# Optimization experiments

Measured on AMD Instinct MI355X. Metric: run time of the kernel, lower is better.

Reference implementation:

```python
import jax, jax.numpy as jnp
import numpy as np

M, N, D = 4, 65536, 256

def setup_inputs() -> dict:
    key = jax.random.key(0)
    k1, k2, k3 = jax.random.split(key, 3)
    x = jax.random.normal(k1, (M, N, D), dtype=jnp.float32)
    # W[i,j] is the (out,in) weight of fusion_layers[i][j]; b[i,j] its bias.
    W = jax.random.normal(k2, (M, M, D, D), dtype=jnp.float32) * (1.0 / np.sqrt(D))
    b = jax.random.normal(k3, (M, M, D), dtype=jnp.float32) * 0.02
    return {"x": x, "W": W, "b": b}

def reference(x, W, b):
    # x: [M, N, D] stacked modality features (zip(*features) rows vectorized over N)
    # out[i] = x[i] + sum_{j != i} (x[j] @ W[i,j]^T + b[i,j])
    m = x.shape[0]
    mask = (1.0 - jnp.eye(m)).astype(x.dtype)            # zero on diagonal (skip i==j)
    y = jnp.einsum('ijef,jnf->ijne', W, x) + b[:, :, None, :]  # [M, M, N, D]
    out = x + jnp.einsum('ij,ijne->ine', mask, y)         # fused masked accumulation
    return out
```

## Files before the change

### kernel.cpp

```cpp
#include <hip/hip_runtime.h>
#include <hip/hip_bf16.h>
#include <stdint.h>

#define NN 65536
#define DD 256

typedef uint32_t u32;
typedef __attribute__((ext_vector_type(4))) float f32x4;
typedef __attribute__((ext_vector_type(4))) u32 u32x4;
typedef __attribute__((ext_vector_type(2))) u32 u32x2;
typedef __attribute__((ext_vector_type(8))) short s16x8;

__device__ inline unsigned short f2bf(float f) {
    union { float f; u32 u; } v; v.f = f;
    u32 u = v.u;
    return (unsigned short)((u + 0x7fffu + ((u >> 16) & 1u)) >> 16);
}

__device__ inline void gl2lds16(const void* g, void* s) {
    __builtin_amdgcn_global_load_lds(
        (const __attribute__((address_space(1))) void*)g,
        (__attribute__((address_space(3))) void*)s, 16, 0, 0);
}

__global__ void prep_w256(const float* __restrict__ W, unsigned short* __restrict__ Wimg) {
    int t = blockIdx.x * blockDim.x + threadIdx.x;
    int E = t * 4;
    int tile = E >> 14;
    int pin = E & 16383;
    int col = pin >> 6;
    int r2e = pin & 63;
    int ct = tile >> 4;
    int j = (tile >> 2) & 3;
    int kk = tile & 3;
    int kl = r2e ^ ((col & 7) << 3);
    int i = ct;
    int e = col;
    int f = kk * 64 + kl;
    u32 p0, p1;
    if (i == j) {
        unsigned short d0 = (e == f + 0) ? 0x3F80 : 0;
        unsigned short d1 = (e == f + 1) ? 0x3F80 : 0;
        unsigned short d2 = (e == f + 2) ? 0x3F80 : 0;
        unsigned short d3 = (e == f + 3) ? 0x3F80 : 0;
        p0 = (u32)d0 | ((u32)d1 << 16);
        p1 = (u32)d2 | ((u32)d3 << 16);
    } else {
        f32x4 w = *(const f32x4*)(W + ((size_t)((i * 4 + j) * 256 + e) << 8) + f);
        p0 = (u32)f2bf(w[0]) | ((u32)f2bf(w[1]) << 16);
        p1 = (u32)f2bf(w[2]) | ((u32)f2bf(w[3]) << 16);
    }
    u32x2 pr = {p0, p1};
    *(u32x2*)(Wimg + E) = pr;
}

__global__ void prep_w128(const float* __restrict__ W, unsigned short* __restrict__ Wimg) {
    int t = blockIdx.x * blockDim.x + threadIdx.x;
    int E = t * 4;
    int tile = E >> 13;
    int pin = E & 8191;
    int col = pin >> 6;
    int r2e = pin & 63;
    int ct = tile >> 4;
    int j = (tile >> 2) & 3;
    int kk = tile & 3;
    int kl = r2e ^ ((col & 7) << 3);
    int c = ct * 128 + col;
    int i = c >> 8, e = c & 255;
    int f = kk * 64 + kl;
    u32 p0, p1;
    if (i == j) {
        p0 = 0u; p1 = 0u;
    } else {
        f32x4 w = *(const f32x4*)(W + ((size_t)((i * 4 + j) * 256 + e) << 8) + f);
        p0 = (u32)f2bf(w[0]) | ((u32)f2bf(w[1]) << 16);
        p1 = (u32)f2bf(w[2]) | ((u32)f2bf(w[3]) << 16);
    }
    u32x2 pr = {p0, p1};
    *(u32x2*)(Wimg + E) = pr;
}

__global__ void prep_x(const float* __restrict__ x, unsigned short* __restrict__ Ximg) {
    int t = blockIdx.x * blockDim.x + threadIdx.x;
    long long E = (long long)t * 4;
    int tile = (int)(E >> 14);
    int pin = (int)(E & 16383);
    int row = pin >> 6;
    int r2e = pin & 63;
    int kk = tile & 3;
    int rt = (tile >> 2) & 255;
    int j = tile >> 10;
    int kl = r2e ^ ((row & 7) << 3);
    int n = rt * 256 + row;
    int f = kk * 64 + kl;
    f32x4 v = *(const f32x4*)(x + ((size_t)j * NN + n) * DD + f);
    u32 p0 = (u32)f2bf(v[0]) | ((u32)f2bf(v[1]) << 16);
    u32 p1 = (u32)f2bf(v[2]) | ((u32)f2bf(v[3]) << 16);
    u32x2 pr = {p0, p1};
    *(u32x2*)(Ximg + E) = pr;
}

__global__ void prep_b(const float* __restrict__ b, float* __restrict__ bsum) {
    int c = blockIdx.x * blockDim.x + threadIdx.x;
    if (c >= 1024) return;
    int i = c >> 8, e = c & 255;
    float s = 0.0f;
    #pragma unroll
    for (int j = 0; j < 4; ++j)
        if (j != i) s += b[((i * 4 + j) << 8) + e];
    bsum[c] = s;
}

__global__ __launch_bounds__(512, 2) void fusion_gemm6(
    const unsigned short* __restrict__ Wimg, const unsigned short* __restrict__ Ximg,
    const float* __restrict__ bsum, float* __restrict__ out) {
    __shared__ __attribute__((aligned(16))) char lds[2][65536];

    const int tid = threadIdx.x;
    const int bid = blockIdx.x;
    const int xcd = bid & 7;
    const int slot = bid >> 3;
    const int ct = slot & 3;
    const int rhi = slot >> 2;
    const int rtile = rhi * 8 + xcd;
    const int n0 = rtile * 256;
    const int col0 = ct * 256;

    const int lane = tid & 63;
    const int wid = tid >> 6;
    const int wm = wid & 1;
    const int wn = wid >> 1;

    f32x4 acc[8][4];
    #pragma unroll
    for (int a = 0; a < 8; ++a)
        #pragma unroll
        for (int b2 = 0; b2 < 4; ++b2)
            acc[a][b2] = (f32x4){0.f, 0.f, 0.f, 0.f};

    const char* WimgB = (const char*)Wimg;
    const char* XimgB = (const char*)Ximg;
    const u32 loff = (u32)(wid * 1024);
    const u32 goff = (u32)(wid * 1024 + lane * 16);

    s16x8 fA0[2][4], fA1[2][4];
    s16x8 fB0[2][2], fB1[2][2];

#define STAGE_TILE(t_, D_)                                                            \
    {                                                                                 \
        int j_ = (t_) >> 2;                                                           \
        int kk_ = (t_) & 3;                                                           \
        const char* as_ = XimgB + (((size_t)((j_ * 256 + rtile) * 4 + kk_)) << 15) + goff; \
        const char* bs_ = WimgB + (((size_t)((ct * 4 + j_) * 4 + kk_)) << 15) + goff; \
        _Pragma("unroll")                                                             \
        for (int q = 0; q < 4; ++q) {                                                 \
            gl2lds16(as_ + q * 8192, (D_) + q * 8192 + loff);                         \
            gl2lds16(bs_ + q * 8192, (D_) + 32768 + q * 8192 + loff);                 \
        }                                                                             \
    }

#define RD_A(BUF_, mh_, SET_)                                                         \
    _Pragma("unroll")                                                                 \
    for (int kh = 0; kh < 2; ++kh) {                                                  \
        _Pragma("unroll")                                                             \
        for (int fm = 0; fm < 4; ++fm) {                                              \
            int r_ = wm * 128 + ((mh_) * 4 + fm) * 16 + (lane & 15);                  \
            u32 o_ = (u32)(r_ * 128 + kh * 64 + (lane >> 4) * 16);                    \
            o_ ^= (u32)((r_ & 7) << 4);                                               \
            SET_[kh][fm] = *(const s16x8*)((BUF_) + o_);                              \
        }                                                                             \
    }

#define RD_B(BUF_, nh_, SET_)                                                         \
    _Pragma("unroll")                                                                 \
    for (int kh = 0; kh < 2; ++kh) {                                                  \
        _Pragma("unroll")                                                             \
        for (int fn = 0; fn < 2; ++fn) {                                              \
            int c_ = wn * 64 + ((nh_) * 2 + fn) * 16 + (lane & 15);                   \
            u32 o_ = (u32)(c_ * 128 + kh * 64 + (lane >> 4) * 16);                    \
            o_ ^= (u32)((c_ & 7) << 4);                                               \
            SET_[kh][fn] = *(const s16x8*)((BUF_) + 32768 + o_);                      \
        }                                                                             \
    }

#define MM(AS_, BS_, mh_, nh_)                                                        \
    _Pragma("unroll")                                                                 \
    for (int kh = 0; kh < 2; ++kh) {                                                  \
        _Pragma("unroll")                                                             \
        for (int fm = 0; fm < 4; ++fm) {                                              \
            _Pragma("unroll")                                                         \
            for (int fn = 0; fn < 2; ++fn) {                                          \
                acc[(mh_) * 4 + fm][(nh_) * 2 + fn] =                                 \
                    __builtin_amdgcn_mfma_f32_16x16x32_bf16(                          \
                        AS_[kh][fm], BS_[kh][fn],                                     \
                        acc[(mh_) * 4 + fm][(nh_) * 2 + fn], 0, 0, 0);                \
            }                                                                         \
        }                                                                             \
    }

    STAGE_TILE(0, lds[0]);
    asm volatile("s_waitcnt vmcnt(0)" ::: "memory");
    __builtin_amdgcn_s_barrier();

    #pragma unroll 1
    for (int t = 0; t < 16; ++t) {
        const char* Bf = lds[t & 1];
        char* Of = lds[(t + 1) & 1];

        if (t < 15) STAGE_TILE(t + 1, Of);

        RD_A(Bf, 0, fA0);
        RD_B(Bf, 0, fB0);
        __builtin_amdgcn_s_setprio(1);
        MM(fA0, fB0, 0, 0);
        RD_B(Bf, 1, fB1);
        MM(fA0, fB1, 0, 1);
        RD_A(Bf, 1, fA1);
        MM(fA1, fB1, 1, 1);
        MM(fA1, fB0, 1, 0);
        __builtin_amdgcn_s_setprio(0);

        asm volatile("s_waitcnt vmcnt(0)" ::: "memory");
        __builtin_amdgcn_s_barrier();
    }

#undef STAGE_TILE
#undef RD_A
#undef RD_B
#undef MM

    const int r0 = (lane >> 4) * 4;
    const int cl = lane & 15;
    #pragma unroll
    for (int mf = 0; mf < 8; ++mf) {
        #pragma unroll
        for (int nf = 0; nf < 4; ++nf) {
            int col_l = wn * 64 + nf * 16 + cl;
            float bs = bsum[col0 + col_l];
            #pragma unroll
            for (int r = 0; r < 4; ++r) {
                int n = n0 + wm * 128 + mf * 16 + r0 + r;
                size_t oidx = ((size_t)ct * NN + n) * DD + col_l;
                out[oidx] = acc[mf][nf][r] + bs;
            }
        }
    }
}

__global__ __launch_bounds__(256, 2) void fusion_gemm_fb(
    const float* __restrict__ x, const unsigned short* __restrict__ Wimg,
    const float* __restrict__ bsum, float* __restrict__ out) {
    __shared__ __attribute__((aligned(16))) unsigned short Alds[128 * 64];
    __shared__ __attribute__((aligned(16))) unsigned short Blds[2][128 * 64];

    const int tid = threadIdx.x;
    const int bid = blockIdx.x;
    const int xcd = bid & 7;
    const int slot = bid >> 3;
    const int ct = slot & 7;
    const int rhi = slot >> 3;
    const int rtile = rhi * 8 + xcd;
    const int n0 = rtile * 128;
    const int col0 = ct * 128;
    const int i = ct >> 1;

    const int lane = tid & 63;
    const int wid = tid >> 6;
    const int wm = wid >> 1;
    const int wn = wid & 1;

    f32x4 acc[4][4];
    #pragma unroll
    for (int a = 0; a < 4; ++a)
        #pragma unroll
        for (int b2 = 0; b2 < 4; ++b2)
            acc[a][b2] = (f32x4){0.f, 0.f, 0.f, 0.f};

    const int sr = tid >> 1;
    const int sh = tid & 1;
    char* Ab = (char*)Alds;
    const char* WimgB = (const char*)Wimg;

    f32x4 av[8];
    {
        int j0 = (i == 0) ? 1 : 0;
        const float* asrc = x + (size_t)j0 * ((size_t)NN * DD) + (size_t)(n0 + sr) * DD + sh * 32;
        #pragma unroll
        for (int q = 0; q < 8; ++q) av[q] = *(const f32x4*)(asrc + q * 4);
        const char* base = WimgB + (((size_t)(ct * 4 + j0) * 4 + 0) << 14) + wid * 1024 + lane * 16;
        char* lb = (char*)Blds[0] + wid * 1024;
        #pragma unroll
        for (int q = 0; q < 4; ++q) gl2lds16(base + q * 4096, lb + q * 4096);
    }

    for (int t = 0; t < 12; ++t) {
        __syncthreads();
        #pragma unroll
        for (int q = 0; q < 4; ++q) {
            f32x4 v0 = av[2 * q], v1 = av[2 * q + 1];
            u32x4 p;
            p[0] = (u32)f2bf(v0[0]) | ((u32)f2bf(v0[1]) << 16);
            p[1] = (u32)f2bf(v0[2]) | ((u32)f2bf(v0[3]) << 16);
            p[2] = (u32)f2bf(v1[0]) | ((u32)f2bf(v1[1]) << 16);
            p[3] = (u32)f2bf(v1[2]) | ((u32)f2bf(v1[3]) << 16);
            u32 o = (u32)(sr * 128 + sh * 64 + q * 16);
            o ^= (u32)((sr & 7) << 4);
            *(u32x4*)(Ab + o) = p;
        }
        __syncthreads();

        if (t < 11) {
            int tn = t + 1;
            int jjn = tn >> 2;
            int jn = jjn + (jjn >= i);
            int kkn = tn & 3;
            const char* base = WimgB + (((size_t)(ct * 4 + jn) * 4 + kkn) << 14) + wid * 1024 + lane * 16;
            char* lb = (char*)Blds[tn & 1] + wid * 1024;
            #pragma unroll
            for (int q = 0; q < 4; ++q) gl2lds16(base + q * 4096, lb + q * 4096);
            const float* asrc = x + (size_t)jn * ((size_t)NN * DD) + (size_t)(n0 + sr) * DD + kkn * 64 + sh * 32;
            #pragma unroll
            for (int q = 0; q < 8; ++q) av[q] = *(const f32x4*)(asrc + q * 4);
        }

        const char* Bb = (const char*)Blds[t & 1];
        #pragma unroll
        for (int kh = 0; kh < 2; ++kh) {
            s16x8 af[4], bfr[4];
            #pragma unroll
            for (int fm = 0; fm < 4; ++fm) {
                int row = wm * 64 + fm * 16 + (lane & 15);
                u32 o = (u32)(row * 128 + kh * 64 + (lane >> 4) * 16);
                o ^= (u32)((row & 7) << 4);
                af[fm] = *(const s16x8*)(Ab + o);
            }
            #pragma unroll
            for (int fn = 0; fn < 4; ++fn) {
                int col = wn * 64 + fn * 16 + (lane & 15);
                u32 o = (u32)(col * 128 + kh * 64 + (lane >> 4) * 16);
                o ^= (u32)((col & 7) << 4);
                bfr[fn] = *(const s16x8*)(Bb + o);
            }
            #pragma unroll
            for (int fm = 0; fm < 4; ++fm)
                #pragma unroll
                for (int fn = 0; fn < 4; ++fn)
                    acc[fm][fn] = __builtin_amdgcn_mfma_f32_16x16x32_bf16(
                        af[fm], bfr[fn], acc[fm][fn], 0, 0, 0);
        }
    }

    const int r0 = (lane >> 4) * 4;
    const int cl = lane & 15;
    #pragma unroll
    for (int fm = 0; fm < 4; ++fm) {
        #pragma unroll
        for (int fn = 0; fn < 4; ++fn) {
            int col_l = wn * 64 + fn * 16 + cl;
            int cglob = col0 + col_l;
            float bs = bsum[cglob];
            int e = cglob & 255;
            #pragma unroll
            for (int r = 0; r < 4; ++r) {
                int row_l = wm * 64 + fm * 16 + r0 + r;
                int n = n0 + row_l;
                size_t oidx = ((size_t)i * NN + n) * DD + e;
                out[oidx] = acc[fm][fn][r] + x[oidx] + bs;
            }
        }
    }
}

extern "C" void kernel_launch(void* const* d_in, const int* in_sizes, int n_in,
                              void* d_out, int out_size, void* d_ws, size_t ws_size,
                              hipStream_t stream) {
    const float* x = (const float*)d_in[0];
    const float* W = (const float*)d_in[1];
    const float* b = (const float*)d_in[2];
    float* out = (float*)d_out;

    unsigned short* Wimg = (unsigned short*)d_ws;
    float* bsum = (float*)((char*)d_ws + ((size_t)8 << 20));
    const size_t ximg_off = (size_t)9 << 20;
    const size_t need = ximg_off + ((size_t)128 << 20);

    if (ws_size >= need) {
        unsigned short* Ximg = (unsigned short*)((char*)d_ws + ximg_off);
        hipLaunchKernelGGL(prep_b, dim3(4), dim3(256), 0, stream, b, bsum);
        hipLaunchKernelGGL(prep_w256, dim3(1024), dim3(256), 0, stream, W, Wimg);
        hipLaunchKernelGGL(prep_x, dim3(65536), dim3(256), 0, stream, x, Ximg);
        hipLaunchKernelGGL(fusion_gemm6, dim3(1024), dim3(512), 0, stream, Wimg, Ximg, bsum, out);
    } else {
        float* bsum2 = (float*)((char*)d_ws + ((size_t)2 << 20));
        hipLaunchKernelGGL(prep_b, dim3(4), dim3(256), 0, stream, b, bsum2);
        hipLaunchKernelGGL(prep_w128, dim3(1024), dim3(256), 0, stream, W, Wimg);
        hipLaunchKernelGGL(fusion_gemm_fb, dim3(4096), dim3(256), 0, stream, x, Wimg, bsum2, out);
    }
}
```

Before: 257.7 us.

## Interleave split A/B staging with MFMA clusters and fine-grained barriers

Splits the global-to-LDS tile staging into separate A and B loads and issues them after the corresponding LDS fragment reads, interleaved with four MFMA clusters per k-step. Adds explicit lgkmcnt waits, sched_barriers and workgroup barriers between clusters so the warps march in lockstep, in the style of a ping-pong schedule. The aim is to spread memory issue across the compute phase and keep the MFMA pipes fed. In exchange it adds more barriers per iteration, which can cost synchronisation stalls. Most of the time goes to the prep kernels, so a gain in the GEMM may be diluted.

After: 267.8 us. +3.9%, slower.

```diff
diff --git a/kernel.cpp b/kernel.cpp
--- a/kernel.cpp
+++ b/kernel.cpp
@@ -111,7 +111,7 @@
     bsum[c] = s;
 }
 
-__global__ __launch_bounds__(512, 2) void fusion_gemm6(
+__global__ __launch_bounds__(512, 2) void fusion_gemm8(
     const unsigned short* __restrict__ Wimg, const unsigned short* __restrict__ Ximg,
     const float* __restrict__ bsum, float* __restrict__ out) {
     __shared__ __attribute__((aligned(16))) char lds[2][65536];
@@ -146,17 +146,24 @@
     s16x8 fA0[2][4], fA1[2][4];
     s16x8 fB0[2][2], fB1[2][2];
 
-#define STAGE_TILE(t_, D_)                                                            \
+#define STAGE_A(t_, D_)                                                               \
     {                                                                                 \
         int j_ = (t_) >> 2;                                                           \
         int kk_ = (t_) & 3;                                                           \
         const char* as_ = XimgB + (((size_t)((j_ * 256 + rtile) * 4 + kk_)) << 15) + goff; \
+        _Pragma("unroll")                                                             \
+        for (int q = 0; q < 4; ++q)                                                   \
+            gl2lds16(as_ + q * 8192, (D_) + q * 8192 + loff);                         \
+    }
+
+#define STAGE_B(t_, D_)                                                               \
+    {                                                                                 \
+        int j_ = (t_) >> 2;                                                           \
+        int kk_ = (t_) & 3;                                                           \
         const char* bs_ = WimgB + (((size_t)((ct * 4 + j_) * 4 + kk_)) << 15) + goff; \
         _Pragma("unroll")                                                             \
-        for (int q = 0; q < 4; ++q) {                                                 \
-            gl2lds16(as_ + q * 8192, (D_) + q * 8192 + loff);                         \
+        for (int q = 0; q < 4; ++q)                                                   \
             gl2lds16(bs_ + q * 8192, (D_) + 32768 + q * 8192 + loff);                 \
-        }                                                                             \
     }
 
 #define RD_A(BUF_, mh_, SET_)                                                         \
@@ -198,36 +205,62 @@
         }                                                                             \
     }
 
-    STAGE_TILE(0, lds[0]);
-    asm volatile("s_waitcnt vmcnt(0)" ::: "memory");
-    __builtin_amdgcn_s_barrier();
+#define SB  __builtin_amdgcn_sched_barrier(0)
+#define BAR __builtin_amdgcn_s_barrier()
+#define LGKM(n_) asm volatile("s_waitcnt lgkmcnt(" #n_ ")" ::: "memory")
+#define VM0 asm volatile("s_waitcnt vmcnt(0)" ::: "memory")
+#define CLUSTER(AS_, BS_, mh_, nh_)                                                   \
+    __builtin_amdgcn_s_setprio(1);                                                    \
+    MM(AS_, BS_, mh_, nh_);                                                           \
+    __builtin_amdgcn_s_setprio(0);                                                    \
+    SB;                                                                               \
+    BAR;
+
+    STAGE_A(0, lds[0]);
+    STAGE_B(0, lds[0]);
+    VM0;
+    BAR;
 
     #pragma unroll 1
     for (int t = 0; t < 16; ++t) {
         const char* Bf = lds[t & 1];
         char* Of = lds[(t + 1) & 1];
 
-        if (t < 15) STAGE_TILE(t + 1, Of);
-
         RD_A(Bf, 0, fA0);
         RD_B(Bf, 0, fB0);
-        __builtin_amdgcn_s_setprio(1);
-        MM(fA0, fB0, 0, 0);
+        if (t < 15) STAGE_A(t + 1, Of);
+        LGKM(8); SB;
+        BAR;
+        LGKM(0); SB;
+        CLUSTER(fA0, fB0, 0, 0);
+
         RD_B(Bf, 1, fB1);
-        MM(fA0, fB1, 0, 1);
+        if (t < 15) STAGE_B(t + 1, Of);
+        BAR;
+        LGKM(0); SB;
+        CLUSTER(fA0, fB1, 0, 1);
+
         RD_A(Bf, 1, fA1);
-        MM(fA1, fB1, 1, 1);
-        MM(fA1, fB0, 1, 0);
-        __builtin_amdgcn_s_setprio(0);
-
-        asm volatile("s_waitcnt vmcnt(0)" ::: "memory");
-        __builtin_amdgcn_s_barrier();
-    }
-
-#undef STAGE_TILE
+        BAR;
+        LGKM(0); SB;
+        CLUSTER(fA1, fB1, 1, 1);
+
+        VM0; SB;
+        BAR;
+        SB;
+        CLUSTER(fA1, fB0, 1, 0);
+    }
+
+#undef STAGE_A
+#undef STAGE_B
 #undef RD_A
 #undef RD_B
 #undef MM
+#undef SB
+#undef BAR
+#undef LGKM
+#undef VM0
+#undef CLUSTER
 
     const int r0 = (lane >> 4) * 4;
     const int cl = lane & 15;
@@ -389,7 +422,7 @@
         hipLaunchKernelGGL(prep_b, dim3(4), dim3(256), 0, stream, b, bsum);
         hipLaunchKernelGGL(prep_w256, dim3(1024), dim3(256), 0, stream, W, Wimg);
         hipLaunchKernelGGL(prep_x, dim3(65536), dim3(256), 0, stream, x, Ximg);
-        hipLaunchKernelGGL(fusion_gemm6, dim3(1024), dim3(512), 0, stream, Wimg, Ximg, bsum, out);
+        hipLaunchKernelGGL(fusion_gemm8, dim3(1024), dim3(512), 0, stream, Wimg, Ximg, bsum, out);
     } else {
         float* bsum2 = (float*)((char*)d_ws + ((size_t)2 << 20));
         hipLaunchKernelGGL(prep_b, dim3(4), dim3(256), 0, stream, b, bsum2);
```

## Fuse fp32-to-bf16 conversion of x into the GEMM A-tile staging

Applied to the files above, without the earlier changes.

Removes the separate prep_x pass that wrote a swizzled bf16 copy of x to workspace. The GEMM now loads fp32 x directly into registers, converts to bf16 and writes the swizzled LDS tile itself, interleaved with the MFMA work of the previous tile. This removes a full read and write pass over x and its large workspace buffer. In exchange the main kernel uses more VGPRs for the fp32 prefetch, does conversion ALU work inside the loop, and reads x from every column-tile block (4x redundant fp32 reads of x versus the bf16 image).

Measured after the change: 557.3 us. 2.16x slower.

```diff
diff --git a/kernel.cpp b/kernel.cpp
--- a/kernel.cpp
+++ b/kernel.cpp
@@ -80,26 +80,6 @@
     *(u32x2*)(Wimg + E) = pr;
 }
 
-__global__ void prep_x(const float* __restrict__ x, unsigned short* __restrict__ Ximg) {
-    int t = blockIdx.x * blockDim.x + threadIdx.x;
-    long long E = (long long)t * 4;
-    int tile = (int)(E >> 14);
-    int pin = (int)(E & 16383);
-    int row = pin >> 6;
-    int r2e = pin & 63;
-    int kk = tile & 3;
-    int rt = (tile >> 2) & 255;
-    int j = tile >> 10;
-    int kl = r2e ^ ((row & 7) << 3);
-    int n = rt * 256 + row;
-    int f = kk * 64 + kl;
-    f32x4 v = *(const f32x4*)(x + ((size_t)j * NN + n) * DD + f);
-    u32 p0 = (u32)f2bf(v[0]) | ((u32)f2bf(v[1]) << 16);
-    u32 p1 = (u32)f2bf(v[2]) | ((u32)f2bf(v[3]) << 16);
-    u32x2 pr = {p0, p1};
-    *(u32x2*)(Ximg + E) = pr;
-}
-
 __global__ void prep_b(const float* __restrict__ b, float* __restrict__ bsum) {
     int c = blockIdx.x * blockDim.x + threadIdx.x;
     if (c >= 1024) return;
@@ -111,8 +91,8 @@
     bsum[c] = s;
 }
 
-__global__ __launch_bounds__(512, 2) void fusion_gemm6(
-    const unsigned short* __restrict__ Wimg, const unsigned short* __restrict__ Ximg,
+__global__ __launch_bounds__(512, 2) void fusion_gemm9(
+    const float* __restrict__ x, const unsigned short* __restrict__ Wimg,
     const float* __restrict__ bsum, float* __restrict__ out) {
     __shared__ __attribute__((aligned(16))) char lds[2][65536];
 
@@ -131,6 +111,9 @@
     const int wm = wid & 1;
     const int wn = wid >> 1;
 
+    const int sr = tid >> 1;
+    const int sh = tid & 1;
+
     f32x4 acc[8][4];
     #pragma unroll
     for (int a = 0; a < 8; ++a)
@@ -139,24 +122,47 @@
             acc[a][b2] = (f32x4){0.f, 0.f, 0.f, 0.f};
 
     const char* WimgB = (const char*)Wimg;
-    const char* XimgB = (const char*)Ximg;
     const u32 loff = (u32)(wid * 1024);
     const u32 goff = (u32)(wid * 1024 + lane * 16);
 
     s16x8 fA0[2][4], fA1[2][4];
     s16x8 fB0[2][2], fB1[2][2];
-
-#define STAGE_TILE(t_, D_)                                                            \
+    f32x4 av[8];
+
+#define LD_AF32(t_)                                                                   \
     {                                                                                 \
         int j_ = (t_) >> 2;                                                           \
         int kk_ = (t_) & 3;                                                           \
-        const char* as_ = XimgB + (((size_t)((j_ * 256 + rtile) * 4 + kk_)) << 15) + goff; \
+        const float* as_ = x + (size_t)j_ * ((size_t)NN * DD)                         \
+                           + (size_t)(n0 + sr) * DD + kk_ * 64 + sh * 32;             \
+        _Pragma("unroll")                                                             \
+        for (int q = 0; q < 8; ++q) av[q] = *(const f32x4*)(as_ + q * 4);             \
+    }
+
+#define CVT_WR_A(D_)                                                                  \
+    {                                                                                 \
+        _Pragma("unroll")                                                             \
+        for (int q = 0; q < 4; ++q) {                                                 \
+            f32x4 v0 = av[2 * q], v1 = av[2 * q + 1];                                 \
+            u32x4 p;                                                                  \
+            p[0] = (u32)f2bf(v0[0]) | ((u32)f2bf(v0[1]) << 16);                       \
+            p[1] = (u32)f2bf(v0[2]) | ((u32)f2bf(v0[3]) << 16);                       \
+            p[2] = (u32)f2bf(v1[0]) | ((u32)f2bf(v1[1]) << 16);                       \
+            p[3] = (u32)f2bf(v1[2]) | ((u32)f2bf(v1[3]) << 16);                       \
+            u32 o_ = (u32)(sr * 128 + sh * 64 + q * 16);                              \
+            o_ ^= (u32)((sr & 7) << 4);                                               \
+            *(u32x4*)((D_) + o_) = p;                                                 \
+        }                                                                             \
+    }
+
+#define STAGE_B(t_, D_)                                                               \
+    {                                                                                 \
+        int j_ = (t_) >> 2;                                                           \
+        int kk_ = (t_) & 3;                                                           \
         const char* bs_ = WimgB + (((size_t)((ct * 4 + j_) * 4 + kk_)) << 15) + goff; \
         _Pragma("unroll")                                                             \
-        for (int q = 0; q < 4; ++q) {                                                 \
-            gl2lds16(as_ + q * 8192, (D_) + q * 8192 + loff);                         \
+        for (int q = 0; q < 4; ++q)                                                   \
             gl2lds16(bs_ + q * 8192, (D_) + 32768 + q * 8192 + loff);                 \
-        }                                                                             \
     }
 
 #define RD_A(BUF_, mh_, SET_)                                                         \
@@ -198,33 +204,49 @@
         }                                                                             \
     }
 
-    STAGE_TILE(0, lds[0]);
+    LD_AF32(0);
+    STAGE_B(0, lds[0]);
+    CVT_WR_A(lds[0]);
+    asm volatile("s_waitcnt lgkmcnt(0)" ::: "memory");
     asm volatile("s_waitcnt vmcnt(0)" ::: "memory");
     __builtin_amdgcn_s_barrier();
+    __builtin_amdgcn_sched_barrier(0);
 
     #pragma unroll 1
     for (int t = 0; t < 16; ++t) {
         const char* Bf = lds[t & 1];
         char* Of = lds[(t + 1) & 1];
 
-        if (t < 15) STAGE_TILE(t + 1, Of);
+        if (t < 15) {
+            LD_AF32(t + 1);
+            STAGE_B(t + 1, Of);
+        }
 
         RD_A(Bf, 0, fA0);
         RD_B(Bf, 0, fB0);
+        RD_B(Bf, 1, fB1);
+        RD_A(Bf, 1, fA1);
         __builtin_amdgcn_s_setprio(1);
         MM(fA0, fB0, 0, 0);
-        RD_B(Bf, 1, fB1);
         MM(fA0, fB1, 0, 1);
-        RD_A(Bf, 1, fA1);
         MM(fA1, fB1, 1, 1);
+        __builtin_amdgcn_s_setprio(0);
+
+        if (t < 15) CVT_WR_A(Of);
+
+        __builtin_amdgcn_s_setprio(1);
         MM(fA1, fB0, 1, 0);
         __builtin_amdgcn_s_setprio(0);
 
+        asm volatile("s_waitcnt lgkmcnt(0)" ::: "memory");
         asm volatile("s_waitcnt vmcnt(0)" ::: "memory");
         __builtin_amdgcn_s_barrier();
-    }
-
-#undef STAGE_TILE
+        __builtin_amdgcn_sched_barrier(0);
+    }
+
+#undef LD_AF32
+#undef CVT_WR_A
+#undef STAGE_B
 #undef RD_A
 #undef RD_B
 #undef MM
@@ -381,15 +403,12 @@
 
     unsigned short* Wimg = (unsigned short*)d_ws;
     float* bsum = (float*)((char*)d_ws + ((size_t)8 << 20));
-    const size_t ximg_off = (size_t)9 << 20;
-    const size_t need = ximg_off + ((size_t)128 << 20);
+    const size_t need = ((size_t)8 << 20) + 4096;
 
     if (ws_size >= need) {
-        unsigned short* Ximg = (unsigned short*)((char*)d_ws + ximg_off);
         hipLaunchKernelGGL(prep_b, dim3(4), dim3(256), 0, stream, b, bsum);
         hipLaunchKernelGGL(prep_w256, dim3(1024), dim3(256), 0, stream, W, Wimg);
-        hipLaunchKernelGGL(prep_x, dim3(65536), dim3(256), 0, stream, x, Ximg);
-        hipLaunchKernelGGL(fusion_gemm6, dim3(1024), dim3(512), 0, stream, Wimg, Ximg, bsum, out);
+        hipLaunchKernelGGL(fusion_gemm9, dim3(1024), dim3(512), 0, stream, x, Wimg, bsum, out);
     } else {
         float* bsum2 = (float*)((char*)d_ws + ((size_t)2 << 20));
         hipLaunchKernelGGL(prep_b, dim3(4), dim3(256), 0, stream, b, bsum2);
```

## Load weight fragments directly from global memory, halve LDS footprint

Applied to the files above, without the earlier changes.

The weight operand is no longer staged through LDS. It is prepared in a plain row-major bf16 layout and each wave loads its B fragments straight from global memory (L2-resident) into registers. Only the activation tile is double-buffered in LDS, which halves shared memory per block and removes one set of LDS writes and reads. Sched barriers are added and the A fragments share a single register set. The trade-off is global-load latency on the MFMA critical path, since B for a tile is read in the same iteration it is consumed, plus uncoalesced 16-byte row reads from L2.

After: 349.4 us. 1.36x slower.

```diff
diff --git a/kernel.cpp b/kernel.cpp
--- a/kernel.cpp
+++ b/kernel.cpp
@@ -23,20 +23,13 @@
         (__attribute__((address_space(3))) void*)s, 16, 0, 0);
 }
 
-__global__ void prep_w256(const float* __restrict__ W, unsigned short* __restrict__ Wimg) {
+__global__ void prep_wbt(const float* __restrict__ W, unsigned short* __restrict__ Wbt) {
     int t = blockIdx.x * blockDim.x + threadIdx.x;
     int E = t * 4;
-    int tile = E >> 14;
-    int pin = E & 16383;
-    int col = pin >> 6;
-    int r2e = pin & 63;
-    int ct = tile >> 4;
-    int j = (tile >> 2) & 3;
-    int kk = tile & 3;
-    int kl = r2e ^ ((col & 7) << 3);
-    int i = ct;
-    int e = col;
-    int f = kk * 64 + kl;
+    int c = E >> 10;
+    int fb = E & 1023;
+    int i = c >> 8, e = c & 255;
+    int j = fb >> 8, f = fb & 255;
     u32 p0, p1;
     if (i == j) {
         unsigned short d0 = (e == f + 0) ? 0x3F80 : 0;
@@ -51,7 +44,7 @@
         p1 = (u32)f2bf(w[2]) | ((u32)f2bf(w[3]) << 16);
     }
     u32x2 pr = {p0, p1};
-    *(u32x2*)(Wimg + E) = pr;
+    *(u32x2*)(Wbt + E) = pr;
 }
 
 __global__ void prep_w128(const float* __restrict__ W, unsigned short* __restrict__ Wimg) {
@@ -111,10 +104,10 @@
     bsum[c] = s;
 }
 
-__global__ __launch_bounds__(512, 2) void fusion_gemm6(
-    const unsigned short* __restrict__ Wimg, const unsigned short* __restrict__ Ximg,
+__global__ __launch_bounds__(512, 2) void fusion_gemm12(
+    const unsigned short* __restrict__ Wbt, const unsigned short* __restrict__ Ximg,
     const float* __restrict__ bsum, float* __restrict__ out) {
-    __shared__ __attribute__((aligned(16))) char lds[2][65536];
+    __shared__ __attribute__((aligned(16))) char lds[2][32768];
 
     const int tid = threadIdx.x;
     const int bid = blockIdx.x;
@@ -138,28 +131,42 @@
         for (int b2 = 0; b2 < 4; ++b2)
             acc[a][b2] = (f32x4){0.f, 0.f, 0.f, 0.f};
 
-    const char* WimgB = (const char*)Wimg;
     const char* XimgB = (const char*)Ximg;
     const u32 loff = (u32)(wid * 1024);
     const u32 goff = (u32)(wid * 1024 + lane * 16);
 
-    s16x8 fA0[2][4], fA1[2][4];
+    const char* WbtB = (const char*)Wbt
+        + ((size_t)(ct * 256 + wn * 64 + (lane & 15)) * 1024 + (size_t)((lane >> 4) * 8)) * 2;
+
+    s16x8 fA[2][4];
     s16x8 fB0[2][2], fB1[2][2];
 
-#define STAGE_TILE(t_, D_)                                                            \
+#define STAGE_A(t_, D_)                                                               \
     {                                                                                 \
         int j_ = (t_) >> 2;                                                           \
         int kk_ = (t_) & 3;                                                           \
         const char* as_ = XimgB + (((size_t)((j_ * 256 + rtile) * 4 + kk_)) << 15) + goff; \
-        const char* bs_ = WimgB + (((size_t)((ct * 4 + j_) * 4 + kk_)) << 15) + goff; \
         _Pragma("unroll")                                                             \
-        for (int q = 0; q < 4; ++q) {                                                 \
+        for (int q = 0; q < 4; ++q)                                                   \
             gl2lds16(as_ + q * 8192, (D_) + q * 8192 + loff);                         \
-            gl2lds16(bs_ + q * 8192, (D_) + 32768 + q * 8192 + loff);                 \
+    }
+
+#define RD_BG(t_, nh_, SET_)                                                          \
+    {                                                                                 \
+        int j_ = (t_) >> 2;                                                           \
+        int kk_ = (t_) & 3;                                                           \
+        _Pragma("unroll")                                                             \
+        for (int kh = 0; kh < 2; ++kh) {                                              \
+            _Pragma("unroll")                                                         \
+            for (int fn = 0; fn < 2; ++fn) {                                          \
+                SET_[kh][fn] = *(const s16x8*)(WbtB                                   \
+                    + ((size_t)(((nh_) * 2 + fn) * 16) * 1024) * 2                    \
+                    + ((size_t)(j_ * 256 + kk_ * 64 + kh * 32)) * 2);                 \
+            }                                                                         \
         }                                                                             \
     }
 
-#define RD_A(BUF_, mh_, SET_)                                                         \
+#define RD_A(BUF_, mh_)                                                               \
     _Pragma("unroll")                                                                 \
     for (int kh = 0; kh < 2; ++kh) {                                                  \
         _Pragma("unroll")                                                             \
@@ -167,23 +174,11 @@
             int r_ = wm * 128 + ((mh_) * 4 + fm) * 16 + (lane & 15);                  \
             u32 o_ = (u32)(r_ * 128 + kh * 64 + (lane >> 4) * 16);                    \
             o_ ^= (u32)((r_ & 7) << 4);                                               \
-            SET_[kh][fm] = *(const s16x8*)((BUF_) + o_);                              \
+            fA[kh][fm] = *(const s16x8*)((BUF_) + o_);                                \
         }                                                                             \
     }
 
-#define RD_B(BUF_, nh_, SET_)                                                         \
-    _Pragma("unroll")                                                                 \
-    for (int kh = 0; kh < 2; ++kh) {                                                  \
-        _Pragma("unroll")                                                             \
-        for (int fn = 0; fn < 2; ++fn) {                                              \
-            int c_ = wn * 64 + ((nh_) * 2 + fn) * 16 + (lane & 15);                   \
-            u32 o_ = (u32)(c_ * 128 + kh * 64 + (lane >> 4) * 16);                    \
-            o_ ^= (u32)((c_ & 7) << 4);                                               \
-            SET_[kh][fn] = *(const s16x8*)((BUF_) + 32768 + o_);                      \
-        }                                                                             \
-    }
-
-#define MM(AS_, BS_, mh_, nh_)                                                        \
+#define MM(BS_, mh_, nh_)                                                             \
     _Pragma("unroll")                                                                 \
     for (int kh = 0; kh < 2; ++kh) {                                                  \
         _Pragma("unroll")                                                             \
@@ -192,41 +187,46 @@
             for (int fn = 0; fn < 2; ++fn) {                                          \
                 acc[(mh_) * 4 + fm][(nh_) * 2 + fn] =                                 \
                     __builtin_amdgcn_mfma_f32_16x16x32_bf16(                          \
-                        AS_[kh][fm], BS_[kh][fn],                                     \
+                        fA[kh][fm], BS_[kh][fn],                                      \
                         acc[(mh_) * 4 + fm][(nh_) * 2 + fn], 0, 0, 0);                \
             }                                                                         \
         }                                                                             \
     }
 
-    STAGE_TILE(0, lds[0]);
+    STAGE_A(0, lds[0]);
     asm volatile("s_waitcnt vmcnt(0)" ::: "memory");
     __builtin_amdgcn_s_barrier();
+    __builtin_amdgcn_sched_barrier(0);
 
     #pragma unroll 1
     for (int t = 0; t < 16; ++t) {
         const char* Bf = lds[t & 1];
         char* Of = lds[(t + 1) & 1];
 
-        if (t < 15) STAGE_TILE(t + 1, Of);
-
-        RD_A(Bf, 0, fA0);
-        RD_B(Bf, 0, fB0);
+        if (t < 15) STAGE_A(t + 1, Of);
+        RD_BG(t, 0, fB0);
+        RD_BG(t, 1, fB1);
+
+        RD_A(Bf, 0);
         __builtin_amdgcn_s_setprio(1);
-        MM(fA0, fB0, 0, 0);
-        RD_B(Bf, 1, fB1);
-        MM(fA0, fB1, 0, 1);
-        RD_A(Bf, 1, fA1);
-        MM(fA1, fB1, 1, 1);
-        MM(fA1, fB0, 1, 0);
+        MM(fB0, 0, 0);
+        MM(fB1, 0, 1);
+        __builtin_amdgcn_s_setprio(0);
+
+        RD_A(Bf, 1);
+        __builtin_amdgcn_s_setprio(1);
+        MM(fB1, 1, 1);
+        MM(fB0, 1, 0);
         __builtin_amdgcn_s_setprio(0);
 
         asm volatile("s_waitcnt vmcnt(0)" ::: "memory");
         __builtin_amdgcn_s_barrier();
-    }
-
-#undef STAGE_TILE
+        __builtin_amdgcn_sched_barrier(0);
+    }
+
+#undef STAGE_A
+#undef RD_BG
 #undef RD_A
-#undef RD_B
 #undef MM
 
     const int r0 = (lane >> 4) * 4;
@@ -379,7 +379,7 @@
     const float* b = (const float*)d_in[2];
     float* out = (float*)d_out;
 
-    unsigned short* Wimg = (unsigned short*)d_ws;
+    unsigned short* Wbuf = (unsigned short*)d_ws;
     float* bsum = (float*)((char*)d_ws + ((size_t)8 << 20));
     const size_t ximg_off = (size_t)9 << 20;
     const size_t need = ximg_off + ((size_t)128 << 20);
@@ -387,13 +387,13 @@
     if (ws_size >= need) {
         unsigned short* Ximg = (unsigned short*)((char*)d_ws + ximg_off);
         hipLaunchKernelGGL(prep_b, dim3(4), dim3(256), 0, stream, b, bsum);
-        hipLaunchKernelGGL(prep_w256, dim3(1024), dim3(256), 0, stream, W, Wimg);
+        hipLaunchKernelGGL(prep_wbt, dim3(1024), dim3(256), 0, stream, W, Wbuf);
         hipLaunchKernelGGL(prep_x, dim3(65536), dim3(256), 0, stream, x, Ximg);
-        hipLaunchKernelGGL(fusion_gemm6, dim3(1024), dim3(512), 0, stream, Wimg, Ximg, bsum, out);
+        hipLaunchKernelGGL(fusion_gemm12, dim3(1024), dim3(512), 0, stream, Wbuf, Ximg, bsum, out);
     } else {
         float* bsum2 = (float*)((char*)d_ws + ((size_t)2 << 20));
         hipLaunchKernelGGL(prep_b, dim3(4), dim3(256), 0, stream, b, bsum2);
-        hipLaunchKernelGGL(prep_w128, dim3(1024), dim3(256), 0, stream, W, Wimg);
-        hipLaunchKernelGGL(fusion_gemm_fb, dim3(4096), dim3(256), 0, stream, x, Wimg, bsum2, out);
-    }
-}
+        hipLaunchKernelGGL(prep_w128, dim3(1024), dim3(256), 0, stream, W, Wbuf);
+        hipLaunchKernelGGL(fusion_gemm_fb, dim3(4096), dim3(256), 0, stream, x, Wbuf, bsum2, out);
+    }
+}
```
